# Optimization experiments

Hardware: AMD Instinct MI355X
Metric: run time of the kernel (lower is better)

Reference implementation:

```python
import jax, jax.numpy as jnp
import numpy as np

B, STATE_DIM, T = 4096, 24, 8
V, D, LAT = 65536, 64, 128
NL, NH, MAXDIM, MEM = 3, 8, 32, 10
FF = 4 * LAT  # dim_feedforward = latent_dim * 4 = 512


def setup_inputs():
    key = jax.random.key(0)
    ks = jax.random.split(key, 20)
    w = lambda i, shape, s=0.02: (jax.random.normal(ks[i], shape, jnp.float32) * s)
    return {
        "dimension_tokens": jax.random.randint(ks[0], (STATE_DIM, T), 0, V),
        "dimension_traits": jax.random.normal(ks[1], (B, STATE_DIM, 2), jnp.float32),
        "rel_goal": jax.random.normal(ks[2], (B, STATE_DIM), jnp.float32),
        "memory_context": jax.random.normal(ks[3], (B, MEM, D), jnp.float32),
        "token_embedding": w(4, (V, D), 1.0),
        "dim_embedding": w(5, (MAXDIM, D), 1.0),
        "trait_W": w(6, (D, 2)), "trait_b": jnp.zeros((D,), jnp.float32),
        "intent_W": w(7, (D, 1)), "intent_b": jnp.zeros((D,), jnp.float32),
        "cls_token": w(8, (1, 1, D), 1.0),
        "Wqkv": w(9, (NL, 3 * D, D)), "bqkv": jnp.zeros((NL, 3 * D), jnp.float32),
        "Wo": w(10, (NL, D, D)), "bo": jnp.zeros((NL, D), jnp.float32),
        "ln1_g": jnp.ones((NL, D), jnp.float32), "ln1_b": jnp.zeros((NL, D), jnp.float32),
        "W1": w(11, (NL, FF, D)), "b1": jnp.zeros((NL, FF), jnp.float32),
        "W2": w(12, (NL, D, FF)), "b2": jnp.zeros((NL, D), jnp.float32),
        "ln2_g": jnp.ones((NL, D), jnp.float32), "ln2_b": jnp.zeros((NL, D), jnp.float32),
        "out_W": w(13, (LAT, D)), "out_b": jnp.zeros((LAT,), jnp.float32),
        "out_ln_g": jnp.ones((LAT,), jnp.float32), "out_ln_b": jnp.zeros((LAT,), jnp.float32),
    }


def _ln(x, g, b, eps=1e-5):
    m = jnp.mean(x, -1, keepdims=True)
    v = jnp.var(x, -1, keepdims=True)
    return (x - m) * jax.lax.rsqrt(v + eps) * g + b


def _mha(x, Wqkv, bqkv, Wo, bo):
    Bb, S, Dd = x.shape
    hd = Dd // NH
    qkv = x @ Wqkv.T + bqkv
    q, k, v = jnp.split(qkv, 3, axis=-1)
    heads = lambda t: t.reshape(Bb, S, NH, hd).transpose(0, 2, 1, 3)
    q, k, v = heads(q), heads(k), heads(v)
    scores = jnp.einsum('bhqd,bhkd->bhqk', q, k) * np.float32(1.0 / np.sqrt(hd))
    attn = jax.nn.softmax(scores, axis=-1)
    out = jnp.einsum('bhqk,bhkd->bhqd', attn, v).transpose(0, 2, 1, 3).reshape(Bb, S, Dd)
    return out @ Wo.T + bo


def reference(dimension_tokens, dimension_traits, rel_goal, memory_context,
              token_embedding, dim_embedding, trait_W, trait_b, intent_W, intent_b,
              cls_token, Wqkv, bqkv, Wo, bo, ln1_g, ln1_b, W1, b1, W2, b2,
              ln2_g, ln2_b, out_W, out_b, out_ln_g, out_ln_b):
    Bb = rel_goal.shape[0]
    state_dim = rel_goal.shape[-1]
    # fused gather + mean-pool over each dimension's token list: [state_dim, D]
    tok = jnp.mean(token_embedding[dimension_tokens], axis=1)
    pos = dim_embedding[:state_dim]                                   # [state_dim, D]
    trait_e = dimension_traits @ trait_W.T + trait_b                  # [B, state_dim, D]
    intent_e = rel_goal[..., None] @ intent_W.T + intent_b            # [B, state_dim, D]
    seq = tok[None] + pos[None] + trait_e + intent_e                  # [B, state_dim, D]
    cls = jnp.broadcast_to(cls_token, (Bb, 1, D))
    x = jnp.concatenate([cls, seq, memory_context], axis=1)           # [B, 1+state_dim+MEM, D]
    # post-LN (norm_first=False) TransformerEncoder, dropout=0 (eval)
    for l in range(NL):
        x = _ln(x + _mha(x, Wqkv[l], bqkv[l], Wo[l], bo[l]), ln1_g[l], ln1_b[l])
        ff = jax.nn.gelu(x @ W1[l].T + b1[l], approximate=False) @ W2[l].T + b2[l]
        x = _ln(x + ff, ln2_g[l], ln2_b[l])
    situation = _ln(x[:, 0] @ out_W.T + out_b, out_ln_g, out_ln_b)    # [B, LAT]
    situation_sequence = x[:, 1:1 + state_dim]                        # [B, state_dim, D]
    cur = jnp.mean(situation_sequence, axis=1, keepdims=True)
    new_memory = jnp.concatenate([memory_context, cur], axis=1)[:, -MEM:]
    return situation, situation_sequence, new_memory
```

## Files before the change

### kernel.cpp

```cpp
#include <hip/hip_runtime.h>

typedef _Float16 f16;
typedef _Float16 f16x2 __attribute__((ext_vector_type(2)));
typedef _Float16 f16x4 __attribute__((ext_vector_type(4)));
typedef _Float16 f16x8 __attribute__((ext_vector_type(8)));
typedef float floatx4 __attribute__((ext_vector_type(4)));

#define MFMA(a, b, c) __builtin_amdgcn_mfma_f32_16x16x32_f16((a), (b), (c), 0, 0, 0)
#define MFMA16(a, b, c) __builtin_amdgcn_mfma_f32_16x16x16f16((a), (b), (c), 0, 0, 0)

constexpr int S = 35;
constexpr int NH = 8;
constexpr int NL = 3;
constexpr int G = 2;
constexpr int RP = 80;
constexpr int MT = 5;
constexpr int BUF = RP * 64;
constexpr int SEQOFF = 4096 * 128;
constexpr int MEMOFF = SEQOFF + 4096 * 24 * 64;
constexpr int TOKPOS_OFF = 245760;
constexpr float QSCL = 0.51006982f;

__device__ __forceinline__ int sw64(int r, int c) {
    return (r << 6) + ((((c >> 3) ^ r) & 7) << 3) + (c & 7);
}
__device__ __forceinline__ int sw128(int r, int c) {
    return (r << 7) + ((((c >> 3) ^ (r & 7))) << 3) + (c & 7);
}

struct Params {
    const int* tok;
    const float *traits, *relg, *mem, *temb, *demb, *traitW, *traitb, *intentW, *intentb, *cls;
    const float *bqkv, *bo, *ln1g, *ln1b, *b1, *b2, *ln2g, *ln2b;
    const float *outW, *outb, *olng, *olnb;
    const f16 *Wqkv, *Wo, *W1, *W2;
    const float* tokpos;
    float* out;
};

__global__ void cvt_all(const float* __restrict__ wqkv, const float* __restrict__ wo,
                        const float* __restrict__ w1, const float* __restrict__ w2,
                        const int* __restrict__ tok, const float* __restrict__ temb,
                        const float* __restrict__ demb, const float* __restrict__ traitb,
                        const float* __restrict__ intentb, f16* __restrict__ dst) {
    if (blockIdx.x == 240) {
        float* tp = (float*)(dst + TOKPOS_OFF);
        for (int idx = threadIdx.x; idx < 24 * 64; idx += 256) {
            int s = idx >> 6, d = idx & 63;
            float a = 0.f;
#pragma unroll
            for (int t = 0; t < 8; ++t) a += temb[tok[s * 8 + t] * 64 + d];
            tp[idx] = a * 0.125f + demb[idx] + traitb[d] + intentb[d];
        }
        return;
    }
    int i = (blockIdx.x * 256 + threadIdx.x) * 4;
    const float* src;
    int off;
    if (i < 36864)       { src = wqkv; off = 0; }
    else if (i < 49152)  { src = wo;   off = 36864; }
    else if (i < 147456) { src = w1;   off = 49152; }
    else                 { src = w2;   off = 147456; }
    floatx4 v = *(const floatx4*)&src[i - off];
    f16x4 o;
    o[0] = (f16)v[0]; o[1] = (f16)v[1]; o[2] = (f16)v[2]; o[3] = (f16)v[3];
    *(f16x4*)&dst[i] = o;
}

__device__ inline f16x4 pack4(float a, float b, float c, float d) {
    f16x2 lo = __builtin_bit_cast(f16x2, __builtin_amdgcn_cvt_pkrtz(a, b));
    f16x2 hi = __builtin_bit_cast(f16x2, __builtin_amdgcn_cvt_pkrtz(c, d));
    f16x4 r; r[0] = lo[0]; r[1] = lo[1]; r[2] = hi[0]; r[3] = hi[1];
    return r;
}

__device__ inline float gelu_f(float x) {
    float x2 = x * x;
    float u = __builtin_fmaf(x2, 0.044715f, 1.0f);
    float xm = x * -2.302585f;
    float z = __builtin_amdgcn_exp2f(xm * u);
    return x * __builtin_amdgcn_rcpf(1.f + z);
}

__device__ inline void ln_row_half(const f16* buf, f16* dst, int row, int half,
                                   const float* g, const float* bb) {
    float v[32];
    float sum = 0.f, sq = 0.f;
    int c0 = half * 32;
#pragma unroll
    for (int kv = 0; kv < 4; ++kv) {
        f16x8 x8 = *(const f16x8*)&buf[sw64(row, c0 + kv * 8)];
#pragma unroll
        for (int e = 0; e < 8; ++e) {
            float f = (float)x8[e];
            v[kv * 8 + e] = f;
            sum += f;
            sq += f * f;
        }
    }
    sum += __shfl_xor(sum, 1, 64);
    sq += __shfl_xor(sq, 1, 64);
    float mean = sum * (1.f / 64.f);
    float var = sq * (1.f / 64.f) - mean * mean;
    float rs = rsqrtf(var + 1e-5f);
#pragma unroll
    for (int kv = 0; kv < 8; ++kv) {
        floatx4 g4 = *(const floatx4*)&g[c0 + kv * 4];
        floatx4 b4 = *(const floatx4*)&bb[c0 + kv * 4];
        *(f16x4*)&dst[sw64(row, c0 + kv * 4)] =
            pack4((v[kv * 4 + 0] - mean) * rs * g4[0] + b4[0],
                  (v[kv * 4 + 1] - mean) * rs * g4[1] + b4[1],
                  (v[kv * 4 + 2] - mean) * rs * g4[2] + b4[2],
                  (v[kv * 4 + 3] - mean) * rs * g4[3] + b4[3]);
    }
}

__global__ __launch_bounds__(256, 4) void fused_tfm_kernel(Params p) {
    __shared__ __align__(16) f16 xlds[BUF];
    __shared__ __align__(16) f16 scratch[3 * BUF];

    f16* qbuf = scratch;
    f16* kbuf = scratch + BUF;
    f16* vbuf = scratch + 2 * BUF;
    f16* hbuf = scratch;

    const int tid = threadIdx.x;
    const int lane = tid & 63;
    const int w = tid >> 6;
    const int l15 = lane & 15;
    const int quad = lane >> 4;
    const int b0 = blockIdx.x * G;

    for (int idx = tid; idx < G * S * 64; idx += 256) {
        int i = idx / (S * 64);
        int rem = idx - i * S * 64;
        int r = rem >> 6, d = rem & 63;
        int b = b0 + i;
        float v;
        if (r == 0) {
            v = p.cls[d];
        } else if (r <= 24) {
            int s = r - 1;
            v = p.tokpos[s * 64 + d] + p.traits[b * 48 + s * 2] * p.traitW[d * 2]
                + p.traits[b * 48 + s * 2 + 1] * p.traitW[d * 2 + 1]
                + p.relg[b * 24 + s] * p.intentW[d];
        } else {
            v = p.mem[b * 640 + (r - 25) * 64 + d];
        }
        xlds[sw64(i * S + r, d)] = (f16)v;
    }
    for (int idx = tid; idx < (RP - G * S) * 64; idx += 256) {
        int r = G * S + (idx >> 6), d = idx & 63;
        xlds[sw64(r, d)] = (f16)0.f;
    }
    __syncthreads();

#pragma unroll 1
    for (int l = 0; l < NL; ++l) {
        const f16* Wqkv_l = p.Wqkv + l * 192 * 64;
        const float* bqkv_l = p.bqkv + l * 192;
        const f16* Wo_l = p.Wo + l * 64 * 64;
        const float* bo_l = p.bo + l * 64;
        const float* ln1g_l = p.ln1g + l * 64;
        const float* ln1b_l = p.ln1b + l * 64;
        const f16* W1_l = p.W1 + l * 512 * 64;
        const float* b1_l = p.b1 + l * 512;
        const f16* W2_l = p.W2 + l * 64 * 512;
        const float* b2_l = p.b2 + l * 64;
        const float* ln2g_l = p.ln2g + l * 64;
        const float* ln2b_l = p.ln2b + l * 64;

        {
            f16x8 xb[MT][2];
#pragma unroll
            for (int m = 0; m < MT; ++m)
#pragma unroll
                for (int kf = 0; kf < 2; ++kf)
                    xb[m][kf] = *(const f16x8*)&xlds[sw64(m * 16 + l15, kf * 32 + quad * 8)];
#pragma unroll
            for (int nt = w; nt < 12; nt += 4) {
                f16x8 wf0 = *(const f16x8*)&Wqkv_l[(nt * 16 + l15) * 64 + quad * 8];
                f16x8 wf1 = *(const f16x8*)&Wqkv_l[(nt * 16 + l15) * 64 + 32 + quad * 8];
                floatx4 bias4 = *(const floatx4*)&bqkv_l[nt * 16 + quad * 4];
                floatx4 acc[MT];
#pragma unroll
                for (int m = 0; m < MT; ++m) {
                    acc[m] = {0.f, 0.f, 0.f, 0.f};
                    acc[m] = MFMA(wf0, xb[m][0], acc[m]);
                    acc[m] = MFMA(wf1, xb[m][1], acc[m]);
                }
                if (nt < 4) {
                    int oc = nt * 16 + quad * 4;
#pragma unroll
                    for (int m = 0; m < MT; ++m) {
                        int row = m * 16 + l15;
                        *(f16x4*)&qbuf[sw64(row, oc)] =
                            pack4((acc[m][0] + bias4[0]) * QSCL, (acc[m][1] + bias4[1]) * QSCL,
                                  (acc[m][2] + bias4[2]) * QSCL, (acc[m][3] + bias4[3]) * QSCL);
                    }
                } else if (nt < 8) {
                    int oc = (nt - 4) * 16 + quad * 4;
#pragma unroll
                    for (int m = 0; m < MT; ++m) {
                        int row = m * 16 + l15;
                        *(f16x4*)&kbuf[sw64(row, oc)] =
                            pack4(acc[m][0] + bias4[0], acc[m][1] + bias4[1],
                                  acc[m][2] + bias4[2], acc[m][3] + bias4[3]);
                    }
                } else {
                    int oc = (nt - 8) * 16 + quad * 4;
#pragma unroll
                    for (int m = 0; m < MT; ++m) {
                        int row = m * 16 + l15;
                        if (row < 70) {
                            int ii = row >= 35 ? 1 : 0;
                            f16* vp = vbuf + ii * 2560 + oc * 40 + (row - ii * 35);
                            vp[0]   = (f16)(acc[m][0] + bias4[0]);
                            vp[40]  = (f16)(acc[m][1] + bias4[1]);
                            vp[80]  = (f16)(acc[m][2] + bias4[2]);
                            vp[120] = (f16)(acc[m][3] + bias4[3]);
                        }
                    }
                }
            }
            if (tid < 128) vbuf[(tid >> 6) * 2560 + (tid & 63) * 40 + 35] = (f16)0.f;
        }
        __syncthreads();

        {
            f16x4 z4 = {};
            floatx4 zf = {0.f, 0.f, 0.f, 0.f};
#pragma unroll 1
            for (int jj = 0; jj < 4; ++jj) {
                int job = w * 4 + jj;
                int i = job >> 3;
                int h = job & 7;
                int rbase = i * S;
                int ccol = h * 8 + (quad & 1) * 4;
                f16x4 kf[3], vf[3], qf[3];
#pragma unroll
                for (int jt = 0; jt < 3; ++jt) {
                    f16x4 t = *(const f16x4*)&kbuf[sw64(rbase + jt * 16 + l15, ccol)];
                    kf[jt] = (quad >= 2) ? z4 : t;
                }
                const f16* vTb = vbuf + i * 2560 + (h * 8 + (l15 & 7)) * 40;
                vf[0] = *(const f16x4*)&vTb[quad * 4];
                vf[1] = *(const f16x4*)&vTb[16 + quad * 4];
                vf[2] = *(const f16x4*)&vTb[32];
#pragma unroll
                for (int qt = 0; qt < 3; ++qt)
                    qf[qt] = *(const f16x4*)&qbuf[sw64(rbase + qt * 16 + l15, ccol)];

#pragma unroll
                for (int qt = 0; qt < 3; ++qt) {
                    floatx4 s0 = MFMA16(kf[0], qf[qt], zf);
                    floatx4 s1 = MFMA16(kf[1], qf[qt], zf);
                    floatx4 s2 = MFMA16(kf[2], qf[qt], zf);
                    float e[12];
                    float lsum = 0.f;
#pragma unroll
                    for (int r = 0; r < 4; ++r) {
                        e[r] = __builtin_amdgcn_exp2f(s0[r]);
                        lsum += e[r];
                    }
#pragma unroll
                    for (int r = 0; r < 4; ++r) {
                        e[4 + r] = __builtin_amdgcn_exp2f(s1[r]);
                        lsum += e[4 + r];
                    }
#pragma unroll
                    for (int r = 0; r < 4; ++r) {
                        float v = __builtin_amdgcn_exp2f(s2[r]);
                        v = (quad == 0 && r < 3) ? v : 0.f;
                        e[8 + r] = v;
                        lsum += v;
                    }
                    f16x4 p0 = pack4(e[0], e[1], e[2], e[3]);
                    f16x4 p1 = pack4(e[4], e[5], e[6], e[7]);
                    f16x4 p2 = pack4(e[8], e[9], e[10], e[11]);
                    floatx4 acc = {0.f, 0.f, 0.f, 0.f};
                    acc = MFMA16(vf[0], p0, acc);
                    acc = MFMA16(vf[1], p1, acc);
                    acc = MFMA16(vf[2], p2, acc);
                    lsum += __shfl_xor(lsum, 16, 64);
                    lsum += __shfl_xor(lsum, 32, 64);
                    float inv = __builtin_amdgcn_rcpf(lsum);
                    if (quad < 2 && (qt < 2 || l15 < 3)) {
                        *(f16x4*)&qbuf[sw64(rbase + qt * 16 + l15, h * 8 + quad * 4)] =
                            pack4(acc[0] * inv, acc[1] * inv, acc[2] * inv, acc[3] * inv);
                    }
                }
            }
        }
        __syncthreads();

        {
            f16x8 ab[MT][2];
#pragma unroll
            for (int m = 0; m < MT; ++m)
#pragma unroll
                for (int kf = 0; kf < 2; ++kf)
                    ab[m][kf] = *(const f16x8*)&qbuf[sw64(m * 16 + l15, kf * 32 + quad * 8)];
            f16x8 wf0 = *(const f16x8*)&Wo_l[(w * 16 + l15) * 64 + quad * 8];
            f16x8 wf1 = *(const f16x8*)&Wo_l[(w * 16 + l15) * 64 + 32 + quad * 8];
            int oc = w * 16 + quad * 4;
            floatx4 bo4 = *(const floatx4*)&bo_l[oc];
            floatx4 oacc[MT];
#pragma unroll
            for (int m = 0; m < MT; ++m) {
                oacc[m] = {0.f, 0.f, 0.f, 0.f};
                oacc[m] = MFMA(wf0, ab[m][0], oacc[m]);
                oacc[m] = MFMA(wf1, ab[m][1], oacc[m]);
            }
#pragma unroll
            for (int m = 0; m < MT; ++m) {
                int row = m * 16 + l15;
                f16x4 res = *(const f16x4*)&xlds[sw64(row, oc)];
                *(f16x4*)&vbuf[sw64(row, oc)] =
                    pack4(oacc[m][0] + bo4[0] + (float)res[0],
                          oacc[m][1] + bo4[1] + (float)res[1],
                          oacc[m][2] + bo4[2] + (float)res[2],
                          oacc[m][3] + bo4[3] + (float)res[3]);
            }
        }
        __syncthreads();

        if (tid < 2 * G * S) ln_row_half(vbuf, xlds, tid >> 1, tid & 1, ln1g_l, ln1b_l);
        __syncthreads();

        {
            f16x8 a2[MT][2];
#pragma unroll
            for (int m = 0; m < MT; ++m)
#pragma unroll
                for (int kf = 0; kf < 2; ++kf)
                    a2[m][kf] = *(const f16x8*)&xlds[sw64(m * 16 + l15, kf * 32 + quad * 8)];
            floatx4 facc[MT];
#pragma unroll
            for (int m = 0; m < MT; ++m) facc[m] = {0.f, 0.f, 0.f, 0.f};

#pragma unroll 1
            for (int c = 0; c < 4; ++c) {
#pragma unroll
                for (int ntl = w; ntl < 8; ntl += 4) {
                    int gc = c * 128 + ntl * 16;
                    f16x8 w1f0 = *(const f16x8*)&W1_l[(gc + l15) * 64 + quad * 8];
                    f16x8 w1f1 = *(const f16x8*)&W1_l[(gc + l15) * 64 + 32 + quad * 8];
                    floatx4 b14 = *(const floatx4*)&b1_l[gc + quad * 4];
                    int oc = ntl * 16 + quad * 4;
                    floatx4 hacc[MT];
#pragma unroll
                    for (int m = 0; m < MT; ++m) {
                        hacc[m] = {0.f, 0.f, 0.f, 0.f};
                        hacc[m] = MFMA(w1f0, a2[m][0], hacc[m]);
                        hacc[m] = MFMA(w1f1, a2[m][1], hacc[m]);
                    }
#pragma unroll
                    for (int m = 0; m < MT; ++m) {
                        int row = m * 16 + l15;
                        *(f16x4*)&hbuf[sw128(row, oc)] =
                            pack4(gelu_f(hacc[m][0] + b14[0]), gelu_f(hacc[m][1] + b14[1]),
                                  gelu_f(hacc[m][2] + b14[2]), gelu_f(hacc[m][3] + b14[3]));
                    }
                }
                __syncthreads();
                f16x8 w2f[4];
#pragma unroll
                for (int kf = 0; kf < 4; ++kf)
                    w2f[kf] = *(const f16x8*)&W2_l[(w * 16 + l15) * 512 + c * 128 + kf * 32 + quad * 8];
#pragma unroll
                for (int m = 0; m < MT; ++m) {
                    f16x8 h0 = *(const f16x8*)&hbuf[sw128(m * 16 + l15, 0 + quad * 8)];
                    f16x8 h1 = *(const f16x8*)&hbuf[sw128(m * 16 + l15, 32 + quad * 8)];
                    f16x8 h2 = *(const f16x8*)&hbuf[sw128(m * 16 + l15, 64 + quad * 8)];
                    f16x8 h3 = *(const f16x8*)&hbuf[sw128(m * 16 + l15, 96 + quad * 8)];
                    facc[m] = MFMA(w2f[0], h0, facc[m]);
                    facc[m] = MFMA(w2f[1], h1, facc[m]);
                    facc[m] = MFMA(w2f[2], h2, facc[m]);
                    facc[m] = MFMA(w2f[3], h3, facc[m]);
                }
                __syncthreads();
            }

            int oc = w * 16 + quad * 4;
            floatx4 b24 = *(const floatx4*)&b2_l[oc];
#pragma unroll
            for (int m = 0; m < MT; ++m) {
                int row = m * 16 + l15;
                f16x4 res = *(const f16x4*)&xlds[sw64(row, oc)];
                *(f16x4*)&vbuf[sw64(row, oc)] =
                    pack4(facc[m][0] + b24[0] + (float)res[0],
                          facc[m][1] + b24[1] + (float)res[1],
                          facc[m][2] + b24[2] + (float)res[2],
                          facc[m][3] + b24[3] + (float)res[3]);
            }
        }
        __syncthreads();

        if (tid < 2 * G * S) ln_row_half(vbuf, xlds, tid >> 1, tid & 1, ln2g_l, ln2b_l);
        __syncthreads();
    }

    float* sitlds = (float*)scratch;
    {
        int i = tid >> 7, j = tid & 127;
        float s = p.outb[j];
#pragma unroll
        for (int kv = 0; kv < 8; ++kv) {
            f16x8 xv = *(const f16x8*)&xlds[sw64(i * S, kv * 8)];
            floatx4 w0 = *(const floatx4*)&p.outW[j * 64 + kv * 8];
            floatx4 w1 = *(const floatx4*)&p.outW[j * 64 + kv * 8 + 4];
#pragma unroll
            for (int e = 0; e < 4; ++e) s += (float)xv[e] * w0[e];
#pragma unroll
            for (int e = 0; e < 4; ++e) s += (float)xv[4 + e] * w1[e];
        }
        sitlds[i * 128 + j] = s;
    }
    __syncthreads();

    if (w < 2) {
        int i = w;
        float v0 = sitlds[i * 128 + lane];
        float v1 = sitlds[i * 128 + 64 + lane];
        float sum = v0 + v1, sq = v0 * v0 + v1 * v1;
#pragma unroll
        for (int off = 32; off >= 1; off >>= 1) {
            sum += __shfl_xor(sum, off, 64);
            sq += __shfl_xor(sq, off, 64);
        }
        float mean = sum * (1.f / 128.f);
        float rs = rsqrtf(sq * (1.f / 128.f) - mean * mean + 1e-5f);
        int b = b0 + i;
        __builtin_nontemporal_store((v0 - mean) * rs * p.olng[lane] + p.olnb[lane],
                                    &p.out[b * 128 + lane]);
        __builtin_nontemporal_store((v1 - mean) * rs * p.olng[64 + lane] + p.olnb[64 + lane],
                                    &p.out[b * 128 + 64 + lane]);
    }

    for (int pp = tid; pp < G * 384; pp += 256) {
        int i = pp / 384;
        int q = pp - i * 384;
        int s = q >> 4, dp = (q & 15) * 4;
        int b = b0 + i;
        f16x4 xv = *(const f16x4*)&xlds[sw64(i * S + 1 + s, dp)];
        floatx4 o = {(float)xv[0], (float)xv[1], (float)xv[2], (float)xv[3]};
        __builtin_nontemporal_store(o, (floatx4*)&p.out[SEQOFF + b * 1536 + s * 64 + dp]);
    }
    for (int pp = tid; pp < G * 144; pp += 256) {
        int i = pp / 144;
        int q = pp - i * 144;
        int mr = q >> 4, dp = (q & 15) * 4;
        int b = b0 + i;
        floatx4 v = *(const floatx4*)&p.mem[b * 640 + (1 + mr) * 64 + dp];
        __builtin_nontemporal_store(v, (floatx4*)&p.out[MEMOFF + b * 640 + mr * 64 + dp]);
    }
    if (tid < G * 64) {
        int i = tid >> 6, d = tid & 63;
        float s = 0.f;
#pragma unroll
        for (int sr = 0; sr < 24; ++sr) s += (float)xlds[sw64(i * S + 1 + sr, d)];
        __builtin_nontemporal_store(s * (1.f / 24.f), &p.out[MEMOFF + (b0 + i) * 640 + 576 + d]);
    }
}

extern "C" void kernel_launch(void* const* d_in, const int* in_sizes, int n_in,
                              void* d_out, int out_size, void* d_ws, size_t ws_size,
                              hipStream_t stream) {
    (void)in_sizes; (void)n_in; (void)out_size; (void)ws_size;

    f16* ws = (f16*)d_ws;
    hipLaunchKernelGGL(cvt_all, dim3(241), dim3(256), 0, stream,
                       (const float*)d_in[11], (const float*)d_in[13],
                       (const float*)d_in[17], (const float*)d_in[19],
                       (const int*)d_in[0], (const float*)d_in[4],
                       (const float*)d_in[5], (const float*)d_in[7],
                       (const float*)d_in[9], ws);

    Params p;
    p.tok = (const int*)d_in[0];
    p.traits = (const float*)d_in[1];
    p.relg = (const float*)d_in[2];
    p.mem = (const float*)d_in[3];
    p.temb = (const float*)d_in[4];
    p.demb = (const float*)d_in[5];
    p.traitW = (const float*)d_in[6];
    p.traitb = (const float*)d_in[7];
    p.intentW = (const float*)d_in[8];
    p.intentb = (const float*)d_in[9];
    p.cls = (const float*)d_in[10];
    p.bqkv = (const float*)d_in[12];
    p.bo = (const float*)d_in[14];
    p.ln1g = (const float*)d_in[15];
    p.ln1b = (const float*)d_in[16];
    p.b1 = (const float*)d_in[18];
    p.b2 = (const float*)d_in[20];
    p.ln2g = (const float*)d_in[21];
    p.ln2b = (const float*)d_in[22];
    p.outW = (const float*)d_in[23];
    p.outb = (const float*)d_in[24];
    p.olng = (const float*)d_in[25];
    p.olnb = (const float*)d_in[26];
    p.Wqkv = ws;
    p.Wo = ws + 36864;
    p.W1 = ws + 49152;
    p.W2 = ws + 147456;
    p.tokpos = (const float*)(ws + TOKPOS_OFF);
    p.out = (float*)d_out;

    hipLaunchKernelGGL(fused_tfm_kernel, dim3(4096 / G), dim3(256), 0, stream, p);
}
```

Measured before the change: 414.6 us.

## Double-buffer FFN hidden chunks, fold Q scale into weights, defer softmax normalization

The FFN loop is restructured into 64-wide hidden chunks with ping-pong LDS buffers. Each iteration computes the next chunk's W1+GELU while consuming the current chunk in W2, so only one barrier per chunk is needed instead of two. The Q scaling is folded into the converted Wqkv weights. Softmax normalization is deferred: per-row reciprocal sums go to LDS and are applied after the output projection, taking the rcp off the attention critical path. The cost is extra LDS use for the row sums and a larger unroll in the attention loop.

```diff
diff --git a/kernel.cpp b/kernel.cpp
--- a/kernel.cpp
+++ b/kernel.cpp
@@ -24,9 +24,6 @@
 __device__ __forceinline__ int sw64(int r, int c) {
     return (r << 6) + ((((c >> 3) ^ r) & 7) << 3) + (c & 7);
 }
-__device__ __forceinline__ int sw128(int r, int c) {
-    return (r << 7) + ((((c >> 3) ^ (r & 7))) << 3) + (c & 7);
-}
 
 struct Params {
     const int* tok;
@@ -57,13 +54,16 @@
     int i = (blockIdx.x * 256 + threadIdx.x) * 4;
     const float* src;
     int off;
-    if (i < 36864)       { src = wqkv; off = 0; }
+    float scl = 1.f;
+    if (i < 36864)       { src = wqkv; off = 0;
+                           if (((i >> 6) % 192) < 64) scl = QSCL; }
     else if (i < 49152)  { src = wo;   off = 36864; }
     else if (i < 147456) { src = w1;   off = 49152; }
     else                 { src = w2;   off = 147456; }
     floatx4 v = *(const floatx4*)&src[i - off];
     f16x4 o;
-    o[0] = (f16)v[0]; o[1] = (f16)v[1]; o[2] = (f16)v[2]; o[3] = (f16)v[3];
+    o[0] = (f16)(v[0] * scl); o[1] = (f16)(v[1] * scl);
+    o[2] = (f16)(v[2] * scl); o[3] = (f16)(v[3] * scl);
     *(f16x4*)&dst[i] = o;
 }
 
@@ -122,7 +122,8 @@
     f16* qbuf = scratch;
     f16* kbuf = scratch + BUF;
     f16* vbuf = scratch + 2 * BUF;
-    f16* hbuf = scratch;
+    f16* hA = scratch;
+    f16* hB = scratch + BUF;
 
     const int tid = threadIdx.x;
     const int lane = tid & 63;
@@ -191,12 +192,13 @@
                 }
                 if (nt < 4) {
                     int oc = nt * 16 + quad * 4;
+                    floatx4 bq = bias4 * QSCL;
 #pragma unroll
                     for (int m = 0; m < MT; ++m) {
                         int row = m * 16 + l15;
                         *(f16x4*)&qbuf[sw64(row, oc)] =
-                            pack4((acc[m][0] + bias4[0]) * QSCL, (acc[m][1] + bias4[1]) * QSCL,
-                                  (acc[m][2] + bias4[2]) * QSCL, (acc[m][3] + bias4[3]) * QSCL);
+                            pack4(acc[m][0] + bq[0], acc[m][1] + bq[1],
+                                  acc[m][2] + bq[2], acc[m][3] + bq[3]);
                     }
                 } else if (nt < 8) {
                     int oc = (nt - 4) * 16 + quad * 4;
@@ -230,7 +232,8 @@
         {
             f16x4 z4 = {};
             floatx4 zf = {0.f, 0.f, 0.f, 0.f};
-#pragma unroll 1
+            float* linv = (float*)&xlds[70 * 64];
+#pragma unroll 2
             for (int jj = 0; jj < 4; ++jj) {
                 int job = w * 4 + jj;
                 int i = job >> 3;
@@ -282,19 +285,21 @@
                     acc = MFMA16(vf[0], p0, acc);
                     acc = MFMA16(vf[1], p1, acc);
                     acc = MFMA16(vf[2], p2, acc);
+                    if (quad < 2 && (qt < 2 || l15 < 3)) {
+                        *(f16x4*)&qbuf[sw64(rbase + qt * 16 + l15, h * 8 + quad * 4)] =
+                            pack4(acc[0], acc[1], acc[2], acc[3]);
+                    }
                     lsum += __shfl_xor(lsum, 16, 64);
                     lsum += __shfl_xor(lsum, 32, 64);
-                    float inv = __builtin_amdgcn_rcpf(lsum);
-                    if (quad < 2 && (qt < 2 || l15 < 3)) {
-                        *(f16x4*)&qbuf[sw64(rbase + qt * 16 + l15, h * 8 + quad * 4)] =
-                            pack4(acc[0] * inv, acc[1] * inv, acc[2] * inv, acc[3] * inv);
-                    }
+                    if (quad == 0 && (qt < 2 || l15 < 3))
+                        linv[rbase + qt * 16 + l15] = __builtin_amdgcn_rcpf(lsum);
                 }
             }
         }
         __syncthreads();
 
         {
+            const float* linv = (const float*)&xlds[70 * 64];
             f16x8 ab[MT][2];
 #pragma unroll
             for (int m = 0; m < MT; ++m)
@@ -315,12 +320,13 @@
 #pragma unroll
             for (int m = 0; m < MT; ++m) {
                 int row = m * 16 + l15;
+                float iv = linv[row];
                 f16x4 res = *(const f16x4*)&xlds[sw64(row, oc)];
                 *(f16x4*)&vbuf[sw64(row, oc)] =
-                    pack4(oacc[m][0] + bo4[0] + (float)res[0],
-                          oacc[m][1] + bo4[1] + (float)res[1],
-                          oacc[m][2] + bo4[2] + (float)res[2],
-                          oacc[m][3] + bo4[3] + (float)res[3]);
+                    pack4(oacc[m][0] * iv + bo4[0] + (float)res[0],
+                          oacc[m][1] * iv + bo4[1] + (float)res[1],
+                          oacc[m][2] * iv + bo4[2] + (float)res[2],
+                          oacc[m][3] * iv + bo4[3] + (float)res[3]);
             }
         }
         __syncthreads();
@@ -339,50 +345,76 @@
 #pragma unroll
             for (int m = 0; m < MT; ++m) facc[m] = {0.f, 0.f, 0.f, 0.f};
 
+            const int oc = w * 16 + quad * 4;
+
+            {
+                int gc = w * 16;
+                f16x8 w1f0 = *(const f16x8*)&W1_l[(gc + l15) * 64 + quad * 8];
+                f16x8 w1f1 = *(const f16x8*)&W1_l[(gc + l15) * 64 + 32 + quad * 8];
+                floatx4 b14 = *(const floatx4*)&b1_l[gc + quad * 4];
+                floatx4 hacc[MT];
+#pragma unroll
+                for (int m = 0; m < MT; ++m) {
+                    hacc[m] = {0.f, 0.f, 0.f, 0.f};
+                    hacc[m] = MFMA(w1f0, a2[m][0], hacc[m]);
+                    hacc[m] = MFMA(w1f1, a2[m][1], hacc[m]);
+                }
+#pragma unroll
+                for (int m = 0; m < MT; ++m) {
+                    int row = m * 16 + l15;
+                    *(f16x4*)&hA[sw64(row, oc)] =
+                        pack4(gelu_f(hacc[m][0] + b14[0]), gelu_f(hacc[m][1] + b14[1]),
+                              gelu_f(hacc[m][2] + b14[2]), gelu_f(hacc[m][3] + b14[3]));
+                }
+            }
+            __syncthreads();
+
 #pragma unroll 1
-            for (int c = 0; c < 4; ++c) {
-#pragma unroll
-                for (int ntl = w; ntl < 8; ntl += 4) {
-                    int gc = c * 128 + ntl * 16;
-                    f16x8 w1f0 = *(const f16x8*)&W1_l[(gc + l15) * 64 + quad * 8];
-                    f16x8 w1f1 = *(const f16x8*)&W1_l[(gc + l15) * 64 + 32 + quad * 8];
-                    floatx4 b14 = *(const floatx4*)&b1_l[gc + quad * 4];
-                    int oc = ntl * 16 + quad * 4;
-                    floatx4 hacc[MT];
-#pragma unroll
-                    for (int m = 0; m < MT; ++m) {
-                        hacc[m] = {0.f, 0.f, 0.f, 0.f};
-                        hacc[m] = MFMA(w1f0, a2[m][0], hacc[m]);
-                        hacc[m] = MFMA(w1f1, a2[m][1], hacc[m]);
-                    }
-#pragma unroll
-                    for (int m = 0; m < MT; ++m) {
-                        int row = m * 16 + l15;
-                        *(f16x4*)&hbuf[sw128(row, oc)] =
-                            pack4(gelu_f(hacc[m][0] + b14[0]), gelu_f(hacc[m][1] + b14[1]),
-                                  gelu_f(hacc[m][2] + b14[2]), gelu_f(hacc[m][3] + b14[3]));
-                    }
+            for (int c = 0; c < 7; ++c) {
+                f16* cb = (c & 1) ? hB : hA;
+                f16* nb = (c & 1) ? hA : hB;
+                int gc = (c + 1) * 64 + w * 16;
+                f16x8 w1f0 = *(const f16x8*)&W1_l[(gc + l15) * 64 + quad * 8];
+                f16x8 w1f1 = *(const f16x8*)&W1_l[(gc + l15) * 64 + 32 + quad * 8];
+                f16x8 w2f0 = *(const f16x8*)&W2_l[(w * 16 + l15) * 512 + c * 64 + quad * 8];
+                f16x8 w2f1 = *(const f16x8*)&W2_l[(w * 16 + l15) * 512 + c * 64 + 32 + quad * 8];
+                floatx4 b14 = *(const floatx4*)&b1_l[gc + quad * 4];
+                floatx4 hacc[MT];
+#pragma unroll
+                for (int m = 0; m < MT; ++m) {
+                    hacc[m] = {0.f, 0.f, 0.f, 0.f};
+                    hacc[m] = MFMA(w1f0, a2[m][0], hacc[m]);
+                    hacc[m] = MFMA(w1f1, a2[m][1], hacc[m]);
+                }
+#pragma unroll
+                for (int m = 0; m < MT; ++m) {
+                    f16x8 h0 = *(const f16x8*)&cb[sw64(m * 16 + l15, quad * 8)];
+                    f16x8 h1 = *(const f16x8*)&cb[sw64(m * 16 + l15, 32 + quad * 8)];
+                    facc[m] = MFMA(w2f0, h0, facc[m]);
+                    facc[m] = MFMA(w2f1, h1, facc[m]);
+                }
+#pragma unroll
+                for (int m = 0; m < MT; ++m) {
+                    int row = m * 16 + l15;
+                    *(f16x4*)&nb[sw64(row, oc)] =
+                        pack4(gelu_f(hacc[m][0] + b14[0]), gelu_f(hacc[m][1] + b14[1]),
+                              gelu_f(hacc[m][2] + b14[2]), gelu_f(hacc[m][3] + b14[3]));
                 }
                 __syncthreads();
-                f16x8 w2f[4];
-#pragma unroll
-                for (int kf = 0; kf < 4; ++kf)
-                    w2f[kf] = *(const f16x8*)&W2_l[(w * 16 + l15) * 512 + c * 128 + kf * 32 + quad * 8];
-#pragma unroll
-                for (int m = 0; m < MT; ++m) {
-                    f16x8 h0 = *(const f16x8*)&hbuf[sw128(m * 16 + l15, 0 + quad * 8)];
-                    f16x8 h1 = *(const f16x8*)&hbuf[sw128(m * 16 + l15, 32 + quad * 8)];
-                    f16x8 h2 = *(const f16x8*)&hbuf[sw128(m * 16 + l15, 64 + quad * 8)];
-                    f16x8 h3 = *(const f16x8*)&hbuf[sw128(m * 16 + l15, 96 + quad * 8)];
-                    facc[m] = MFMA(w2f[0], h0, facc[m]);
-                    facc[m] = MFMA(w2f[1], h1, facc[m]);
-                    facc[m] = MFMA(w2f[2], h2, facc[m]);
-                    facc[m] = MFMA(w2f[3], h3, facc[m]);
-                }
-                __syncthreads();
-            }
-
-            int oc = w * 16 + quad * 4;
+            }
+
+            {
+                f16x8 w2f0 = *(const f16x8*)&W2_l[(w * 16 + l15) * 512 + 448 + quad * 8];
+                f16x8 w2f1 = *(const f16x8*)&W2_l[(w * 16 + l15) * 512 + 448 + 32 + quad * 8];
+#pragma unroll
+                for (int m = 0; m < MT; ++m) {
+                    f16x8 h0 = *(const f16x8*)&hB[sw64(m * 16 + l15, quad * 8)];
+                    f16x8 h1 = *(const f16x8*)&hB[sw64(m * 16 + l15, 32 + quad * 8)];
+                    facc[m] = MFMA(w2f0, h0, facc[m]);
+                    facc[m] = MFMA(w2f1, h1, facc[m]);
+                }
+            }
+
             floatx4 b24 = *(const floatx4*)&b2_l[oc];
 #pragma unroll
             for (int m = 0; m < MT; ++m) {
```

New measurement: 469.5 us. +13.2%, slower.
